# Kernel optimization log

Measured on AMD Instinct MI355X. Metric: run time of the kernel, lower is better.

## Reference

```python
import jax, jax.numpy as jnp
import numpy as np

N_GAUSS = 1536
WIDTH, HEIGHT = 160, 128
FX = FY = 146.44        # 2343.024 * (160/2560)
CX, CY = WIDTH / 2.0, HEIGHT / 2.0
EPS2D = 0.3             # 2D covariance dilation (as in prepare_rasterization_coefficients)
NEAR, FAR = 0.01, 1e10


def eval_sh_basis(dirs):
    # real SH basis up to degree 3, 16 components (matches eval_sh_old)
    x, y, z = dirs[..., 0], dirs[..., 1], dirs[..., 2]
    one = jnp.ones_like(x)
    return jnp.stack([
        0.282095 * one,
        -0.488603 * y, 0.488603 * z, -0.488603 * x,
        1.092548 * x * y, -1.092548 * y * z, 0.315392 * (3 * z * z - 1),
        -1.092548 * x * z, 0.546274 * (x * x - y * y),
        -0.590044 * y * (3 * x * x - y * y), 2.890611 * x * y * z,
        -0.457046 * y * (5 * z * z - 1), 0.373176 * z * (5 * z * z - 3),
        -0.457046 * x * (5 * z * z - 1), 1.445306 * z * (x * x - y * y),
        -0.590044 * x * (x * x - 3 * y * y)], axis=-1)


def quat_to_rot(q):
    q = q / jnp.linalg.norm(q, axis=1, keepdims=True)
    w, x, y, z = q[:, 0], q[:, 1], q[:, 2], q[:, 3]
    R = jnp.stack([
        1 - 2 * (y * y + z * z), 2 * (x * y - z * w), 2 * (x * z + y * w),
        2 * (x * y + z * w), 1 - 2 * (x * x + z * z), 2 * (y * z - x * w),
        2 * (x * z - y * w), 2 * (y * z + x * w), 1 - 2 * (x * x + y * y)], axis=-1)
    return R.reshape(-1, 3, 3)


def get_viewmat(c2w):
    # c2w: (B,3,4); flip y/z camera axes then invert (matches torch get_viewmat)
    R = c2w[:, :3, :3] * jnp.array([[[1.0, -1.0, -1.0]]], dtype=c2w.dtype)
    t = c2w[:, :3, 3:4]
    R_inv = jnp.swapaxes(R, 1, 2)
    t_inv = -(R_inv @ t)
    return R_inv[0], t_inv[0, :, 0]


def setup_inputs() -> dict:
    key = jax.random.key(0)
    k0, k1, k2, k3, k4, k5 = jax.random.split(key, 6)
    N = N_GAUSS
    xy = jax.random.normal(k0, (N, 2), dtype=jnp.float32) * 0.5
    # world z negative -> positive camera-frame depth after axis flip
    z = -(1.0 + 4.0 * jax.random.uniform(k1, (N, 1), dtype=jnp.float32))
    means = jnp.concatenate([xy, z], axis=1)
    quats = jax.random.normal(k2, (N, 4), dtype=jnp.float32)
    log_scales = jax.random.normal(k3, (N, 3), dtype=jnp.float32) * 0.3 - 3.0
    opacity_logits = jax.random.normal(k4, (N,), dtype=jnp.float32)
    sh_coeffs = jax.random.normal(k5, (N, 16, 3), dtype=jnp.float32) * 0.3
    camera_to_worlds = jnp.eye(4, dtype=jnp.float32)[None, :3, :]
    return {"means": means, "quats": quats, "log_scales": log_scales,
            "opacity_logits": opacity_logits, "sh_coeffs": sh_coeffs,
            "camera_to_worlds": camera_to_worlds}


def reference(means, quats, log_scales, opacity_logits, sh_coeffs, camera_to_worlds):
    R_w2c, t_w2c = get_viewmat(camera_to_worlds)
    means_cam = means @ R_w2c.T + t_w2c                    # (N,3)
    depth = means_cam[:, 2]
    mask = (depth > NEAR) & (depth < FAR)

    # view-dependent colors from SH (degree 3)
    cam_pos = camera_to_worlds[0, :3, 3]
    dirs = means - cam_pos
    dirs = dirs / jnp.linalg.norm(dirs, axis=1, keepdims=True)
    colors = jnp.maximum(jnp.einsum('nk,nkc->nc', eval_sh_basis(dirs), sh_coeffs) + 0.5, 0.0)

    # 3D covariance -> camera frame -> EWA 2D projection
    Rg = quat_to_rot(quats)                                 # (N,3,3)
    M = Rg * jnp.exp(log_scales)[:, None, :]                # R @ diag(S)
    cov3d = M @ jnp.swapaxes(M, 1, 2)
    cov_cam = jnp.einsum('ij,njk,lk->nil', R_w2c, cov3d, R_w2c)
    tx, ty, tz = means_cam[:, 0], means_cam[:, 1], means_cam[:, 2]
    rz = 1.0 / tz
    zero = jnp.zeros_like(rz)
    J = jnp.stack([jnp.stack([FX * rz, zero, -FX * tx * rz * rz], -1),
                   jnp.stack([zero, FY * rz, -FY * ty * rz * rz], -1)], -2)  # (N,2,3)
    cov2d = jnp.einsum('nij,njk,nlk->nil', J, cov_cam, J)
    a = cov2d[:, 0, 0] + EPS2D
    c = cov2d[:, 1, 1] + EPS2D
    b = cov2d[:, 0, 1]
    det = a * c - b * b
    A, B, C = c / det, -b / det, a / det                    # conic (inverse 2D cov)

    u = FX * tx * rz + CX
    v = FY * ty * rz + CY
    opac = jax.nn.sigmoid(opacity_logits)

    px = jnp.arange(WIDTH, dtype=means.dtype)
    py = jnp.arange(HEIGHT, dtype=means.dtype)
    dx = px[None, None, :] - u[:, None, None]               # (N,1,W)
    dy = py[None, :, None] - v[:, None, None]               # (N,H,1)
    power = (-0.5 * (A[:, None, None] * dx * dx + C[:, None, None] * dy * dy)
             - B[:, None, None] * (dx * dy))                # (N,H,W)
    alpha = jnp.minimum(0.999, opac[:, None, None] * jnp.exp(power))
    alpha = jnp.where(mask[:, None, None], alpha, 0.0)

    # global depth sort (front-to-back alpha compositing)
    order = jnp.argsort(jnp.where(mask, depth, jnp.inf))
    alpha = alpha[order]
    colors = colors[order]
    T = jnp.cumprod(1.0 - alpha, axis=0)
    T_excl = jnp.concatenate([jnp.ones_like(T[:1]), T[:-1]], axis=0)
    w = T_excl * alpha                                      # (N,H,W)
    rgb = jnp.einsum('nhw,nc->hwc', w, colors)              # (H,W,3)
    return rgb
```

## Files before the change

kernel.cpp:

```cpp
#include <hip/hip_runtime.h>
#include <math.h>

#define N_GAUSS 1536
#define WIDTH   160
#define HEIGHT  128
#define NPIX    (WIDTH * HEIGHT)
#define FXC     146.44f
#define FYC     146.44f
#define CXC     80.0f
#define CYC     64.0f
#define EPS2D   0.3f
#define NEARP   0.01f
#define FARP    1e10f
#define L2E     1.4426950408889634f
#define LN2     0.6931471805599453f
#define CULL_E  25.0f

#define PREP_BLOCKS 384
#define PREP_TPB    256
#define SCAN_LEN4   (N_GAUSS / 64 / 4)

#define NWAVE   16
#define RCHUNK  (N_GAUSS / NWAVE)
#define RPIX    64
#define TILE_W  8
#define TILE_H  8
#define TILES_X (WIDTH / TILE_W)
#define TILES_Y (HEIGHT / TILE_H)

__device__ __forceinline__ float fast_exp2(float x) {
    return __builtin_amdgcn_exp2f(x);
}


__global__ __launch_bounds__(PREP_TPB) void prep_sort_kernel(
    const float* __restrict__ means, const float* __restrict__ quats,
    const float* __restrict__ log_scales, const float* __restrict__ opac_logits,
    const float* __restrict__ sh, const float* __restrict__ c2w,
    float4* __restrict__ bbox, float4* __restrict__ rec)
{
    __shared__ float4 k4_lds[N_GAUSS / 4];
    float* k_lds = (float*)k4_lds;

    float C[12];
#pragma unroll
    for (int k = 0; k < 12; k++) C[k] = c2w[k];
    float R00 =  C[0], R01 =  C[4], R02 =  C[8];
    float R10 = -C[1], R11 = -C[5], R12 = -C[9];
    float R20 = -C[2], R21 = -C[6], R22 = -C[10];
    float cpx = C[3], cpy = C[7], cpz = C[11];
    float t0 = -(R00 * cpx + R01 * cpy + R02 * cpz);
    float t1 = -(R10 * cpx + R11 * cpy + R12 * cpz);
    float t2 = -(R20 * cpx + R21 * cpy + R22 * cpz);

    for (int j = threadIdx.x; j < N_GAUSS; j += PREP_TPB) {
        float mx = means[3 * j], my = means[3 * j + 1], mz = means[3 * j + 2];
        float tzj = R20 * mx + R21 * my + R22 * mz + t2;
        bool m = (tzj > NEARP) && (tzj < FARP);
        k_lds[j] = m ? tzj : INFINITY;
    }
    __syncthreads();

    int i    = blockIdx.x * 4 + (threadIdx.x >> 6);
    int part = threadIdx.x & 63;

    float mx = means[3 * i], my = means[3 * i + 1], mz = means[3 * i + 2];
    float4 qv = ((const float4*)quats)[i];
    float lsx = log_scales[3 * i + 0];
    float lsy = log_scales[3 * i + 1];
    float lsz = log_scales[3 * i + 2];
    float olog = opac_logits[i];
    const float4* sh4 = (const float4*)(sh + i * 48);
    float4 S[12];
#pragma unroll
    for (int k = 0; k < 12; k++) S[k] = sh4[k];
    const float* shf = (const float*)S;

    float tx = R00 * mx + R01 * my + R02 * mz + t0;
    float ty = R10 * mx + R11 * my + R12 * mz + t1;
    float tz = R20 * mx + R21 * my + R22 * mz + t2;
    bool mask = (tz > NEARP) && (tz < FARP);

    float dx = mx - cpx, dy = my - cpy, dz = mz - cpz;
    float rn = rsqrtf(dx * dx + dy * dy + dz * dz);
    float x = dx * rn, y = dy * rn, z = dz * rn;
    float xx = x * x, yy = y * y, zz = z * z;
    float basis[16];
    basis[0]  = 0.282095f;
    basis[1]  = -0.488603f * y;
    basis[2]  = 0.488603f * z;
    basis[3]  = -0.488603f * x;
    basis[4]  = 1.092548f * x * y;
    basis[5]  = -1.092548f * y * z;
    basis[6]  = 0.315392f * (3.f * zz - 1.f);
    basis[7]  = -1.092548f * x * z;
    basis[8]  = 0.546274f * (xx - yy);
    basis[9]  = -0.590044f * y * (3.f * xx - yy);
    basis[10] = 2.890611f * x * y * z;
    basis[11] = -0.457046f * y * (5.f * zz - 1.f);
    basis[12] = 0.373176f * z * (5.f * zz - 3.f);
    basis[13] = -0.457046f * x * (5.f * zz - 1.f);
    basis[14] = 1.445306f * z * (xx - yy);
    basis[15] = -0.590044f * x * (xx - 3.f * yy);
    float cr = 0.f, cg = 0.f, cb = 0.f;
#pragma unroll
    for (int k = 0; k < 16; k++) {
        cr += basis[k] * shf[3 * k + 0];
        cg += basis[k] * shf[3 * k + 1];
        cb += basis[k] * shf[3 * k + 2];
    }
    cr = fmaxf(cr + 0.5f, 0.f);
    cg = fmaxf(cg + 0.5f, 0.f);
    cb = fmaxf(cb + 0.5f, 0.f);

    float qw = qv.x, qx = qv.y, qy = qv.z, qz = qv.w;
    float qn = rsqrtf(qw * qw + qx * qx + qy * qy + qz * qz);
    qw *= qn; qx *= qn; qy *= qn; qz *= qn;
    float sx = expf(lsx);
    float sy = expf(lsy);
    float sz = expf(lsz);
    float M00 = (1.f - 2.f * (qy * qy + qz * qz)) * sx;
    float M01 = (2.f * (qx * qy - qz * qw)) * sy;
    float M02 = (2.f * (qx * qz + qy * qw)) * sz;
    float M10 = (2.f * (qx * qy + qz * qw)) * sx;
    float M11 = (1.f - 2.f * (qx * qx + qz * qz)) * sy;
    float M12 = (2.f * (qy * qz - qx * qw)) * sz;
    float M20 = (2.f * (qx * qz - qy * qw)) * sx;
    float M21 = (2.f * (qy * qz + qx * qw)) * sy;
    float M22 = (1.f - 2.f * (qx * qx + qy * qy)) * sz;
    float V00 = M00 * M00 + M01 * M01 + M02 * M02;
    float V01 = M00 * M10 + M01 * M11 + M02 * M12;
    float V02 = M00 * M20 + M01 * M21 + M02 * M22;
    float V11 = M10 * M10 + M11 * M11 + M12 * M12;
    float V12 = M10 * M20 + M11 * M21 + M12 * M22;
    float V22 = M20 * M20 + M21 * M21 + M22 * M22;

    float T00 = R00 * V00 + R01 * V01 + R02 * V02;
    float T01 = R00 * V01 + R01 * V11 + R02 * V12;
    float T02 = R00 * V02 + R01 * V12 + R02 * V22;
    float T10 = R10 * V00 + R11 * V01 + R12 * V02;
    float T11 = R10 * V01 + R11 * V11 + R12 * V12;
    float T12 = R10 * V02 + R11 * V12 + R12 * V22;
    float T20 = R20 * V00 + R21 * V01 + R22 * V02;
    float T21 = R20 * V01 + R21 * V11 + R22 * V12;
    float T22 = R20 * V02 + R21 * V12 + R22 * V22;
    float cc00 = T00 * R00 + T01 * R01 + T02 * R02;
    float cc01 = T00 * R10 + T01 * R11 + T02 * R12;
    float cc02 = T00 * R20 + T01 * R21 + T02 * R22;
    float cc11 = T10 * R10 + T11 * R11 + T12 * R12;
    float cc12 = T10 * R20 + T11 * R21 + T12 * R22;
    float cc22 = T20 * R20 + T21 * R21 + T22 * R22;

    float rz = 1.f / tz;
    float rz2 = rz * rz;
    float j00 = FXC * rz, j02 = -FXC * tx * rz2;
    float j11 = FYC * rz, j12 = -FYC * ty * rz2;
    float c2d00 = j00 * j00 * cc00 + 2.f * j00 * j02 * cc02 + j02 * j02 * cc22;
    float c2d01 = (j00 * cc01 + j02 * cc12) * j11 + (j00 * cc02 + j02 * cc22) * j12;
    float c2d11 = j11 * j11 * cc11 + 2.f * j11 * j12 * cc12 + j12 * j12 * cc22;

    float a = c2d00 + EPS2D, c = c2d11 + EPS2D, b = c2d01;
    float idet = 1.f / (a * c - b * b);
    float Ac = c * idet, Bc = -b * idet, Cc = a * idet;
    float u = FXC * tx * rz + CXC;
    float v = FYC * ty * rz + CYC;
    float op = 1.f / (1.f + expf(-olog));
    float a2 = -0.5f * L2E * Ac;
    float b2 = -L2E * Bc;
    float c2 = -0.5f * L2E * Cc;
    float o2 = log2f(op);

    float Qmax = fmaxf(0.f, 2.f * LN2 * (CULL_E + o2));
    float rx = sqrtf(Qmax * a);
    float ry = sqrtf(Qmax * c);

    if (!mask) {
        u = 1e30f; v = 1e30f; rx = 0.f; ry = 0.f;
        a2 = 0.f; b2 = 0.f; c2 = 0.f; o2 = -INFINITY;
    }

    float ki = k_lds[i];
    int rank = 0;
    int base4 = part * SCAN_LEN4;
#pragma unroll
    for (int jj = 0; jj < SCAN_LEN4; jj++) {
        int j4 = base4 + jj;
        float4 kk = k4_lds[j4];
        int j = 4 * j4;
        rank += (kk.x < ki) || (kk.x == ki && (j + 0) < i);
        rank += (kk.y < ki) || (kk.y == ki && (j + 1) < i);
        rank += (kk.z < ki) || (kk.z == ki && (j + 2) < i);
        rank += (kk.w < ki) || (kk.w == ki && (j + 3) < i);
    }
    rank += __shfl_xor(rank, 1);
    rank += __shfl_xor(rank, 2);
    rank += __shfl_xor(rank, 4);
    rank += __shfl_xor(rank, 8);
    rank += __shfl_xor(rank, 16);
    rank += __shfl_xor(rank, 32);

    if (part == 0) {
        bbox[rank]        = make_float4(u, v, rx, ry);
        rec[2 * rank]     = make_float4(a2, b2, c2, o2);
        rec[2 * rank + 1] = make_float4(cr, cg, cb, 0.f);
    }
}

__global__ __launch_bounds__(1024) void raster_kernel(
    const float4* __restrict__ bbox, const float4* __restrict__ rec,
    float* __restrict__ out)
{
    __shared__ float4 part_lds[NWAVE * RPIX];

    int wave = __builtin_amdgcn_readfirstlane(threadIdx.x >> 6);
    int lane = threadIdx.x & 63;

    int tile = blockIdx.x;
    int tx0 = (tile % TILES_X) * TILE_W;
    int ty0 = (tile / TILES_X) * TILE_H;
    float px = (float)(tx0 + (lane & 7));
    float py = (float)(ty0 + (lane >> 3));
    float tcx = (float)tx0 + 3.5f;
    float tcy = (float)ty0 + 3.5f;

    int g0 = wave * RCHUNK;

    float T = 1.f, cr = 0.f, cg = 0.f, cb = 0.f;
#pragma unroll
    for (int bseg = 0; bseg < 2; bseg++) {
        int gbase = g0 + (bseg ? 64 : 0);
        int bn    = bseg ? 32 : 64;
        float4 bb = bbox[gbase + (lane < bn ? lane : 0)];
        bool ok = (lane < bn) &&
                  (fabsf(tcx - bb.x) <= bb.z + 3.5f) &&
                  (fabsf(tcy - bb.y) <= bb.w + 3.5f);
        unsigned long long m = __ballot(ok);
        while (m) {
            int bl = __ffsll(m) - 1;
            m &= m - 1;
            float u = __shfl(bb.x, bl);
            float v = __shfl(bb.y, bl);
            int g = gbase + bl;
            float4 f1 = rec[2 * g];
            float4 f2 = rec[2 * g + 1];
            float dx = px - u;
            float dy = py - v;
            float t  = f1.x * dx;
            t = fmaf(f1.y, dy, t);
            float q  = f1.z * dy;
            float pw = fmaf(t, dx, f1.w);
            pw = fmaf(q, dy, pw);
            float alpha = fminf(0.999f, fast_exp2(pw));
            float w = T * alpha;
            cr = fmaf(w, f2.x, cr);
            cg = fmaf(w, f2.y, cg);
            cb = fmaf(w, f2.z, cb);
            T -= w;
        }
    }
    part_lds[wave * RPIX + lane] = make_float4(cr, cg, cb, T);
    __syncthreads();

    if (threadIdx.x < RPIX) {
        int l = threadIdx.x;
        int p = (ty0 + (l >> 3)) * WIDTH + tx0 + (l & 7);
        float Tt = 1.f, r = 0.f, g = 0.f, b = 0.f;
#pragma unroll
        for (int c = 0; c < NWAVE; c++) {
            float4 q = part_lds[c * RPIX + l];
            r = fmaf(Tt, q.x, r);
            g = fmaf(Tt, q.y, g);
            b = fmaf(Tt, q.z, b);
            Tt *= q.w;
        }
        out[3 * p + 0] = r;
        out[3 * p + 1] = g;
        out[3 * p + 2] = b;
    }
}

extern "C" void kernel_launch(void* const* d_in, const int* in_sizes, int n_in,
                              void* d_out, int out_size, void* d_ws, size_t ws_size,
                              hipStream_t stream) {
    const float* means       = (const float*)d_in[0];
    const float* quats       = (const float*)d_in[1];
    const float* log_scales  = (const float*)d_in[2];
    const float* opac_logits = (const float*)d_in[3];
    const float* sh          = (const float*)d_in[4];
    const float* c2w         = (const float*)d_in[5];

    float* ws = (float*)d_ws;
    float4* bbox = (float4*)ws;
    float4* rec  = (float4*)(ws + N_GAUSS * 4);

    prep_sort_kernel<<<PREP_BLOCKS, PREP_TPB, 0, stream>>>(
        means, quats, log_scales, opac_logits, sh, c2w, bbox, rec);
    raster_kernel<<<TILES_X * TILES_Y, NWAVE * 64, 0, stream>>>(
        bbox, rec, (float*)d_out);
}
```

Baseline: 78.12 us.

## Process two tiles per block and repack gaussian records into three float4s

The raster kernel now launches 256 blocks, and the first 64 blocks each handle a second tile, covering all 320 tiles without a second wave of blocks on the 256-CU device. The per-gaussian record is repacked so u and v sit alongside the conic terms, which removes the cross-lane shuffles for the position. Both bbox segments are loaded and balloted up front. In exchange, each record now takes three float4 loads instead of two. A quarter of the blocks also do twice the work, which may lengthen the critical path instead of shortening it.

New measurement: 79.01 us. Within noise of the previous version (+1.1%).

```diff
diff --git a/kernel.cpp b/kernel.cpp
--- a/kernel.cpp
+++ b/kernel.cpp
@@ -27,6 +27,8 @@
 #define TILE_H  8
 #define TILES_X (WIDTH / TILE_W)
 #define TILES_Y (HEIGHT / TILE_H)
+#define NTILES  (TILES_X * TILES_Y)
+#define RBLOCKS 256
 
 __device__ __forceinline__ float fast_exp2(float x) {
     return __builtin_amdgcn_exp2f(x);
@@ -201,8 +203,9 @@
 
     if (part == 0) {
         bbox[rank]        = make_float4(u, v, rx, ry);
-        rec[2 * rank]     = make_float4(a2, b2, c2, o2);
-        rec[2 * rank + 1] = make_float4(cr, cg, cb, 0.f);
+        rec[3 * rank + 0] = make_float4(u, v, a2, b2);
+        rec[3 * rank + 1] = make_float4(c2, o2, cr, cg);
+        rec[3 * rank + 2] = make_float4(cb, 0.f, 0.f, 0.f);
     }
 }
 
@@ -214,68 +217,75 @@
 
     int wave = __builtin_amdgcn_readfirstlane(threadIdx.x >> 6);
     int lane = threadIdx.x & 63;
-
-    int tile = blockIdx.x;
-    int tx0 = (tile % TILES_X) * TILE_W;
-    int ty0 = (tile / TILES_X) * TILE_H;
-    float px = (float)(tx0 + (lane & 7));
-    float py = (float)(ty0 + (lane >> 3));
-    float tcx = (float)tx0 + 3.5f;
-    float tcy = (float)ty0 + 3.5f;
-
     int g0 = wave * RCHUNK;
 
-    float T = 1.f, cr = 0.f, cg = 0.f, cb = 0.f;
-#pragma unroll
-    for (int bseg = 0; bseg < 2; bseg++) {
-        int gbase = g0 + (bseg ? 64 : 0);
-        int bn    = bseg ? 32 : 64;
-        float4 bb = bbox[gbase + (lane < bn ? lane : 0)];
-        bool ok = (lane < bn) &&
-                  (fabsf(tcx - bb.x) <= bb.z + 3.5f) &&
-                  (fabsf(tcy - bb.y) <= bb.w + 3.5f);
-        unsigned long long m = __ballot(ok);
-        while (m) {
-            int bl = __ffsll(m) - 1;
-            m &= m - 1;
-            float u = __shfl(bb.x, bl);
-            float v = __shfl(bb.y, bl);
-            int g = gbase + bl;
-            float4 f1 = rec[2 * g];
-            float4 f2 = rec[2 * g + 1];
-            float dx = px - u;
-            float dy = py - v;
-            float t  = f1.x * dx;
-            t = fmaf(f1.y, dy, t);
-            float q  = f1.z * dy;
-            float pw = fmaf(t, dx, f1.w);
-            pw = fmaf(q, dy, pw);
-            float alpha = fminf(0.999f, fast_exp2(pw));
-            float w = T * alpha;
-            cr = fmaf(w, f2.x, cr);
-            cg = fmaf(w, f2.y, cg);
-            cb = fmaf(w, f2.z, cb);
-            T -= w;
+    int ntile = (blockIdx.x < NTILES - RBLOCKS) ? 2 : 1;
+    for (int ti = 0; ti < ntile; ti++) {
+        int tile = (ti == 0) ? blockIdx.x : (RBLOCKS + blockIdx.x);
+        int tx0 = (tile % TILES_X) * TILE_W;
+        int ty0 = (tile / TILES_X) * TILE_H;
+        float px = (float)(tx0 + (lane & 7));
+        float py = (float)(ty0 + (lane >> 3));
+        float tcx = (float)tx0 + 3.5f;
+        float tcy = (float)ty0 + 3.5f;
+
+        float4 bb0 = bbox[g0 + lane];
+        float4 bb1 = bbox[g0 + 64 + (lane & 31)];
+        bool ok0 = (fabsf(tcx - bb0.x) <= bb0.z + 3.5f) &&
+                   (fabsf(tcy - bb0.y) <= bb0.w + 3.5f);
+        bool ok1 = (lane < 32) &&
+                   (fabsf(tcx - bb1.x) <= bb1.z + 3.5f) &&
+                   (fabsf(tcy - bb1.y) <= bb1.w + 3.5f);
+        unsigned long long m0 = __ballot(ok0);
+        unsigned long long m1 = __ballot(ok1);
+
+        float T = 1.f, cr = 0.f, cg = 0.f, cb = 0.f;
+#pragma unroll
+        for (int bseg = 0; bseg < 2; bseg++) {
+            unsigned long long m = bseg ? m1 : m0;
+            int gbase = g0 + (bseg ? 64 : 0);
+            while (m) {
+                int bl = __ffsll(m) - 1;
+                m &= m - 1;
+                int g = gbase + bl;
+                float4 f0 = rec[3 * g + 0];
+                float4 f1 = rec[3 * g + 1];
+                float4 f2 = rec[3 * g + 2];
+                float dx = px - f0.x;
+                float dy = py - f0.y;
+                float t  = f0.z * dx;
+                t = fmaf(f0.w, dy, t);
+                float q  = f1.x * dy;
+                float pw = fmaf(t, dx, f1.y);
+                pw = fmaf(q, dy, pw);
+                float alpha = fminf(0.999f, fast_exp2(pw));
+                float w = T * alpha;
+                cr = fmaf(w, f1.z, cr);
+                cg = fmaf(w, f1.w, cg);
+                cb = fmaf(w, f2.x, cb);
+                T -= w;
+            }
         }
-    }
-    part_lds[wave * RPIX + lane] = make_float4(cr, cg, cb, T);
-    __syncthreads();
-
-    if (threadIdx.x < RPIX) {
-        int l = threadIdx.x;
-        int p = (ty0 + (l >> 3)) * WIDTH + tx0 + (l & 7);
-        float Tt = 1.f, r = 0.f, g = 0.f, b = 0.f;
-#pragma unroll
-        for (int c = 0; c < NWAVE; c++) {
-            float4 q = part_lds[c * RPIX + l];
-            r = fmaf(Tt, q.x, r);
-            g = fmaf(Tt, q.y, g);
-            b = fmaf(Tt, q.z, b);
-            Tt *= q.w;
+        part_lds[wave * RPIX + lane] = make_float4(cr, cg, cb, T);
+        __syncthreads();
+
+        if (threadIdx.x < RPIX) {
+            int l = threadIdx.x;
+            int p = (ty0 + (l >> 3)) * WIDTH + tx0 + (l & 7);
+            float Tt = 1.f, r = 0.f, g = 0.f, b = 0.f;
+#pragma unroll
+            for (int c = 0; c < NWAVE; c++) {
+                float4 qq = part_lds[c * RPIX + l];
+                r = fmaf(Tt, qq.x, r);
+                g = fmaf(Tt, qq.y, g);
+                b = fmaf(Tt, qq.z, b);
+                Tt *= qq.w;
+            }
+            out[3 * p + 0] = r;
+            out[3 * p + 1] = g;
+            out[3 * p + 2] = b;
         }
-        out[3 * p + 0] = r;
-        out[3 * p + 1] = g;
-        out[3 * p + 2] = b;
+        if (ti + 1 < ntile) __syncthreads();
     }
 }
 
@@ -295,6 +305,6 @@
 
     prep_sort_kernel<<<PREP_BLOCKS, PREP_TPB, 0, stream>>>(
         means, quats, log_scales, opac_logits, sh, c2w, bbox, rec);
-    raster_kernel<<<TILES_X * TILES_Y, NWAVE * 64, 0, stream>>>(
+    raster_kernel<<<RBLOCKS, NWAVE * 64, 0, stream>>>(
         bbox, rec, (float*)d_out);
 }
```
